# Kernel tuning notes

Hardware: AMD Instinct MI355X
Metric: run time of the kernel (lower is better)

Reference implementation:

```python
import jax, jax.numpy as jnp
import numpy as np


def _pairwise_dist(x, y):
    # x: [b, n, d], y: [b, n, d] -> squared L2 distances [b, n, n]
    xx = jnp.sum(x * x, axis=-1)  # [b, n]
    yy = jnp.sum(y * y, axis=-1)  # [b, n]
    zz = jnp.einsum('bnd,bmd->bnm', x, y)  # [b, n, n]
    return xx[:, :, None] + yy[:, None, :] - 2.0 * zz


def setup_inputs() -> dict:
    key = jax.random.key(0)
    k1, k2 = jax.random.split(key)
    bs, n, d = 4, 8192, 3
    x = jax.random.normal(k1, (bs, n, d), dtype=jnp.float32)
    y = jax.random.normal(k2, (bs, n, d), dtype=jnp.float32)
    return {"x": x, "y": y}


def reference(x, y):
    bs, n_points, _ = x.shape
    dist1 = jnp.sqrt(_pairwise_dist(x, y))  # [b, n, n]
    values1 = jnp.min(dist1, axis=2)        # [b, n] min over y for each x point
    dist2 = jnp.sqrt(_pairwise_dist(y, x))
    values2 = jnp.min(dist2, axis=2)        # min over x for each y point
    a = jnp.sum(values1, axis=1) / n_points
    b = jnp.sum(values2, axis=1) / n_points
    return jnp.sum(a) / bs + jnp.sum(b) / bs
```

## Files before the change

kernel.cpp:

```cpp
#include <hip/hip_runtime.h>
#include <stdint.h>

typedef _Float16 half8 __attribute__((ext_vector_type(8)));
typedef float f32x16 __attribute__((ext_vector_type(16)));

#define NPTS 8192
#define BS 4
#define TOTQ 65536
#define TPB 256
#define NS 4
#define QPB 512
#define NCHUNK 4
#define SLICE (NPTS / NS)

__device__ __forceinline__ float4 f4min(float4 a, float4 b) {
    return make_float4(fminf(a.x, b.x), fminf(a.y, b.y), fminf(a.z, b.z), fminf(a.w, b.w));
}

__device__ __forceinline__ void mk_afrag(float p0, float p1, float p2,
                                         half8* ag0, half8* ag1) {
    _Float16 h0 = (_Float16)p0, h1 = (_Float16)p1, h2 = (_Float16)p2;
    _Float16 l0 = (_Float16)(p0 - (float)h0);
    _Float16 l1 = (_Float16)(p1 - (float)h1);
    _Float16 l2 = (_Float16)(p2 - (float)h2);
    _Float16 t2 = (_Float16)-2.0f;
    _Float16 m0 = t2 * h0, m1 = t2 * h1, m2 = t2 * h2;
    _Float16 n0 = t2 * l0, n1 = t2 * l1, n2 = t2 * l2;
    _Float16 one = (_Float16)1.0f, zz = (_Float16)0.0f;
    *ag0 = (half8){m0, m1, m2, n0, n1, n2, m0, m1};
    *ag1 = (half8){m2, one, one, n0, n1, n2, zz, zz};
}

__device__ __forceinline__ void mk_bfrag(float p0, float p1, float p2,
                                         half8* bg0, half8* bg1) {
    float nt = p0 * p0 + p1 * p1 + p2 * p2;
    _Float16 h0 = (_Float16)p0, h1 = (_Float16)p1, h2 = (_Float16)p2;
    _Float16 l0 = (_Float16)(p0 - (float)h0);
    _Float16 l1 = (_Float16)(p1 - (float)h1);
    _Float16 l2 = (_Float16)(p2 - (float)h2);
    _Float16 nh = (_Float16)nt;
    _Float16 nl = (_Float16)(nt - (float)nh);
    _Float16 zz = (_Float16)0.0f;
    *bg0 = (half8){h0, h1, h2, h0, h1, h2, l0, l1};
    *bg1 = (half8){l2, nh, nl, l0, l1, l2, zz, zz};
}

__global__ __launch_bounds__(TPB, 2) void mfma_min_kernel(const float* __restrict__ x,
                                                          const float* __restrict__ y,
                                                          float* __restrict__ partial) {
    __shared__ __align__(16) char lds[2][16384];
    const int tid = threadIdx.x;
    const int wave = tid >> 6;
    const int l = tid & 63;
    const int chunkid = blockIdx.x / NS;
    const int s = blockIdx.x % NS;
    const int qbase = chunkid * QPB;
    const int dir = qbase >> 15;
    const int b = (qbase >> 13) & 3;
    const int qpt = qbase & (BS * NPTS - 1);
    const int tpt = b * NPTS + s * SLICE;
    const float* qsrc = (dir == 0) ? x : y;
    const float* tsrc = (dir == 0) ? y : x;

    half8 afr0, afr1, afr2, afr3;
    {
        const int row = l & 31;
#define MKA(AF, a)                                                                          \
        {                                                                                   \
            const float* p = qsrc + (size_t)(qpt + (wave * 4 + (a)) * 32 + row) * 3;        \
            half8 g0, g1;                                                                   \
            mk_afrag(p[0], p[1], p[2], &g0, &g1);                                           \
            AF = (l < 32) ? g0 : g1;                                                        \
        }
        MKA(afr0, 0) MKA(afr1, 1) MKA(afr2, 2) MKA(afr3, 3)
#undef MKA
    }

    f32x16 mrun0, mrun1, mrun2, mrun3, zc;
#pragma unroll
    for (int r = 0; r < 16; ++r) {
        mrun0[r] = 3.4e38f; mrun1[r] = 3.4e38f;
        mrun2[r] = 3.4e38f; mrun3[r] = 3.4e38f;
        zc[r] = 0.0f;
    }

    float2 rA, rB, rC;
#define BLOAD(c)                                                                            \
    {                                                                                       \
        const float2* p = (const float2*)(tsrc + (size_t)(tpt + (c) * 512 + tid * 2) * 3);  \
        rA = p[0]; rB = p[1]; rC = p[2];                                                    \
    }
#define BPACK(buf)                                                                          \
    {                                                                                       \
        const int t0 = tid * 2;                                                             \
        const int base = (t0 >> 5) * 1024;                                                  \
        const int r0 = (t0 & 31) * 16;                                                      \
        half8 g0, g1;                                                                       \
        mk_bfrag(rA.x, rA.y, rB.x, &g0, &g1);                                               \
        *(half8*)(&lds[buf][base + r0]) = g0;                                               \
        *(half8*)(&lds[buf][base + 512 + r0]) = g1;                                         \
        mk_bfrag(rB.y, rC.x, rC.y, &g0, &g1);                                               \
        *(half8*)(&lds[buf][base + r0 + 16]) = g0;                                          \
        *(half8*)(&lds[buf][base + 512 + r0 + 16]) = g1;                                    \
    }

#define AGROUP(AF, MR, BB0, BB1)                                                            \
    {                                                                                       \
        f32x16 d0 = __builtin_amdgcn_mfma_f32_32x32x16_f16(AF, BB0, zc, 0, 0, 0);           \
        f32x16 d1 = __builtin_amdgcn_mfma_f32_32x32x16_f16(AF, BB1, zc, 0, 0, 0);           \
        _Pragma("unroll")                                                                   \
        for (int r = 0; r < 16; ++r)                                                        \
            MR[r] = fminf(fminf(MR[r], d0[r]), d1[r]);                          \
    }

#define COMPUTE(BB0, BB1)                                                                   \
    AGROUP(afr0, mrun0, BB0, BB1)                                                           \
    AGROUP(afr1, mrun1, BB0, BB1)                                                           \
    AGROUP(afr2, mrun2, BB0, BB1)                                                           \
    AGROUP(afr3, mrun3, BB0, BB1)

    BLOAD(0)
    BPACK(0)
    __syncthreads();

    int cur = 0;
#pragma unroll 1
    for (int c = 0; c < NCHUNK; ++c) {
        if (c + 1 < NCHUNK) BLOAD(c + 1)
        const char* B = lds[cur];
        half8 bA0 = *(const half8*)(B + l * 16);
        half8 bA1 = *(const half8*)(B + 1024 + l * 16);
        half8 bB0, bB1;
#pragma unroll 1
        for (int p = 0; p < 8; p += 2) {
            bB0 = *(const half8*)(B + (p + 1) * 2048 + l * 16);
            bB1 = *(const half8*)(B + (p + 1) * 2048 + 1024 + l * 16);
            COMPUTE(bA0, bA1);
            int pn = (p + 2) & 7;
            bA0 = *(const half8*)(B + pn * 2048 + l * 16);
            bA1 = *(const half8*)(B + pn * 2048 + 1024 + l * 16);
            COMPUTE(bB0, bB1);
        }
        if (c + 1 < NCHUNK) {
            BPACK(cur ^ 1)
            __syncthreads();
            cur ^= 1;
        }
    }
#undef BLOAD
#undef BPACK
#undef COMPUTE
#undef AGROUP

    __syncthreads();
    float* ep = (float*)(&lds[0][0]);
    const int hi4 = (l >> 5) * 4;
    const int col = l & 31;

#define EPASS(AA, MR)                                                                       \
    {                                                                                       \
        _Pragma("unroll")                                                                   \
        for (int r = 0; r < 16; ++r) {                                                      \
            int row = (r & 3) + 8 * (r >> 2) + hi4;                                         \
            ep[wave * 1152 + row * 36 + col] = MR[r];                                       \
        }                                                                                   \
    }                                                                                       \
    __syncthreads();                                                                        \
    if (tid < 128) {                                                                        \
        const float4* rp = (const float4*)(ep + (tid >> 5) * 1152 + (tid & 31) * 36);       \
        float4 a01 = f4min(rp[0], rp[1]), a23 = f4min(rp[2], rp[3]);                        \
        float4 a45 = f4min(rp[4], rp[5]), a67 = f4min(rp[6], rp[7]);                        \
        float4 t = f4min(f4min(a01, a23), f4min(a45, a67));                                 \
        float m = fminf(fminf(t.x, t.y), fminf(t.z, t.w));                                  \
        partial[(size_t)s * TOTQ + qbase + (tid >> 5) * 128 + (AA) * 32 + (tid & 31)] = m;  \
    }                                                                                       \
    __syncthreads();

    EPASS(0, mrun0)
    EPASS(1, mrun1)
    EPASS(2, mrun2)
    EPASS(3, mrun3)
#undef EPASS
}

__global__ __launch_bounds__(TPB) void combine_mfma_kernel(const float* __restrict__ partial,
                                                           const float* __restrict__ x,
                                                           const float* __restrict__ y,
                                                           float* __restrict__ bsum) {
    int q = blockIdx.x * TPB + threadIdx.x;
    int dir = q >> 15;
    int pidx = q & (BS * NPTS - 1);
    const float* src = (dir == 0) ? x : y;
    float p0 = src[pidx * 3 + 0], p1 = src[pidx * 3 + 1], p2 = src[pidx * 3 + 2];
    float nq = p0 * p0 + p1 * p1 + p2 * p2;

    float m = partial[q];
#pragma unroll
    for (int s = 1; s < NS; ++s)
        m = fminf(m, partial[(size_t)s * TOTQ + q]);
    float d = sqrtf(fmaxf(m + nq, 0.0f));
    __shared__ float red[TPB];
    red[threadIdx.x] = d;
    __syncthreads();
    for (int off = TPB / 2; off > 0; off >>= 1) {
        if (threadIdx.x < off) red[threadIdx.x] += red[threadIdx.x + off];
        __syncthreads();
    }
    if (threadIdx.x == 0) bsum[blockIdx.x] = red[0];
}

__global__ __launch_bounds__(TPB) void final_kernel(const float* __restrict__ bsum,
                                                    float* __restrict__ out) {
    __shared__ float red[TPB];
    red[threadIdx.x] = bsum[threadIdx.x];
    __syncthreads();
    for (int off = TPB / 2; off > 0; off >>= 1) {
        if (threadIdx.x < off) red[threadIdx.x] += red[threadIdx.x + off];
        __syncthreads();
    }
    if (threadIdx.x == 0) out[0] = red[0] * (1.0f / 32768.0f);
}

#define QPT 8
#define QPBF (TPB * QPT)
#define NGROUP (TOTQ / QPBF)
#define FNS 8

__global__ __launch_bounds__(TPB) void pack_kernel(const float* __restrict__ x,
                                                   const float* __restrict__ y,
                                                   float4* __restrict__ px,
                                                   float4* __restrict__ py) {
    int i = blockIdx.x * TPB + threadIdx.x;
    if (i < BS * NPTS) {
        float x0 = x[i * 3 + 0], x1 = x[i * 3 + 1], x2 = x[i * 3 + 2];
        px[i] = make_float4(x0, x1, x2, x0 * x0 + x1 * x1 + x2 * x2);
        float y0 = y[i * 3 + 0], y1 = y[i * 3 + 1], y2 = y[i * 3 + 2];
        py[i] = make_float4(y0, y1, y2, y0 * y0 + y1 * y1 + y2 * y2);
    }
}

__global__ __launch_bounds__(TPB) void chamfer_min_kernel(const float4* __restrict__ px,
                                                          const float4* __restrict__ py,
                                                          float* __restrict__ partial) {
    constexpr int SLICEF = NPTS / FNS;
    __shared__ float4 tile[SLICEF];
    const int t = threadIdx.x;
    const int g = blockIdx.x / FNS;
    const int s = blockIdx.x % FNS;
    const int dir = g >> 4;
    const int b = (g >> 2) & 3;
    const int chunk = g & 3;
    const float4* q  = (dir == 0 ? px : py) + b * NPTS + chunk * QPBF;
    const float4* tg = (dir == 0 ? py : px) + b * NPTS + s * SLICEF;
    float a0[QPT], a1[QPT], a2[QPT], qq[QPT], mv[QPT];
#pragma unroll
    for (int i = 0; i < QPT; ++i) {
        float4 v = q[i * TPB + t];
        a0[i] = -2.0f * v.x; a1[i] = -2.0f * v.y; a2[i] = -2.0f * v.z;
        qq[i] = v.w; mv[i] = 3.4e38f;
    }
#pragma unroll
    for (int i = 0; i < SLICEF / TPB; ++i)
        tile[i * TPB + t] = tg[i * TPB + t];
    __syncthreads();
#pragma unroll 2
    for (int j = 0; j < SLICEF; j += 2) {
        float4 v0 = tile[j], v1 = tile[j + 1];
#pragma unroll
        for (int i = 0; i < QPT; ++i) {
            float d0 = fmaf(a2[i], v0.z, fmaf(a1[i], v0.y, fmaf(a0[i], v0.x, v0.w)));
            float d1 = fmaf(a2[i], v1.z, fmaf(a1[i], v1.y, fmaf(a0[i], v1.x, v1.w)));
            mv[i] = fminf(fminf(mv[i], d0), d1);
        }
    }
    const int qg0 = g * QPBF;
#pragma unroll
    for (int i = 0; i < QPT; ++i)
        partial[(size_t)s * TOTQ + qg0 + i * TPB + t] = mv[i] + qq[i];
}

__global__ __launch_bounds__(TPB) void combine_kernel(const float* __restrict__ partial,
                                                      float* __restrict__ bsum) {
    int idx = blockIdx.x * TPB + threadIdx.x;
    float m = 3.4e38f;
#pragma unroll
    for (int s = 0; s < FNS; ++s)
        m = fminf(m, partial[(size_t)s * TOTQ + idx]);
    float d = sqrtf(fmaxf(m, 0.0f));
    __shared__ float red[TPB];
    red[threadIdx.x] = d;
    __syncthreads();
    for (int off = TPB / 2; off > 0; off >>= 1) {
        if (threadIdx.x < off) red[threadIdx.x] += red[threadIdx.x + off];
        __syncthreads();
    }
    if (threadIdx.x == 0) bsum[blockIdx.x] = red[0];
}

extern "C" void kernel_launch(void* const* d_in, const int* in_sizes, int n_in,
                              void* d_out, int out_size, void* d_ws, size_t ws_size,
                              hipStream_t stream) {
    const float* x = (const float*)d_in[0];
    const float* y = (const float*)d_in[1];
    float* out = (float*)d_out;
    char* ws = (char*)d_ws;

    const size_t off_bs = (size_t)NS * TOTQ * 4;
    const size_t need = off_bs + 1024;

    if (ws_size >= need) {
        float* partial = (float*)ws;
        float* bsum = (float*)(ws + off_bs);
        hipLaunchKernelGGL(mfma_min_kernel, dim3((TOTQ / QPB) * NS), dim3(TPB), 0, stream,
                           x, y, partial);
        hipLaunchKernelGGL(combine_mfma_kernel, dim3(TOTQ / TPB), dim3(TPB), 0, stream,
                           partial, x, y, bsum);
        hipLaunchKernelGGL(final_kernel, dim3(1), dim3(TPB), 0, stream, bsum, out);
    } else {
        float4* px = (float4*)ws;
        float4* py = (float4*)(ws + 512 * 1024);
        float* partial = (float*)(ws + 1024 * 1024);
        float* bsum = (float*)(ws + 1024 * 1024 + (size_t)FNS * TOTQ * 4);
        hipLaunchKernelGGL(pack_kernel, dim3((BS * NPTS + TPB - 1) / TPB), dim3(TPB), 0, stream,
                           x, y, px, py);
        hipLaunchKernelGGL(chamfer_min_kernel, dim3(NGROUP * FNS), dim3(TPB), 0, stream,
                           px, py, partial);
        hipLaunchKernelGGL(combine_kernel, dim3(TOTQ / TPB), dim3(TPB), 0, stream,
                           partial, bsum);
        hipLaunchKernelGGL(final_kernel, dim3(1), dim3(TPB), 0, stream, bsum, out);
    }
}
```

Before: 29.00 us.

## Stage entire target slice into LDS upfront instead of double-buffered chunks

Replaces the four-chunk double-buffered LDS pipeline with a single prologue that loads and packs all 2048 target points into a 64KB LDS buffer. Global loads for two chunks are interleaved with packing, then one barrier precedes an uninterrupted 32-step MFMA loop. This removes the per-chunk barriers and load/pack work inside the compute loop. In exchange, LDS use per block rises from 32KB to 64KB, which may limit blocks per CU to two or fewer. Global load latency is also exposed up front instead of overlapped with compute.

```diff
diff --git a/kernel.cpp b/kernel.cpp
--- a/kernel.cpp
+++ b/kernel.cpp
@@ -10,7 +10,6 @@
 #define TPB 256
 #define NS 4
 #define QPB 512
-#define NCHUNK 4
 #define SLICE (NPTS / NS)
 
 __device__ __forceinline__ float4 f4min(float4 a, float4 b) {
@@ -48,7 +47,7 @@
 __global__ __launch_bounds__(TPB, 2) void mfma_min_kernel(const float* __restrict__ x,
                                                           const float* __restrict__ y,
                                                           float* __restrict__ partial) {
-    __shared__ __align__(16) char lds[2][16384];
+    __shared__ __align__(16) char lds[65536];
     const int tid = threadIdx.x;
     const int wave = tid >> 6;
     const int l = tid & 63;
@@ -84,25 +83,36 @@
         zc[r] = 0.0f;
     }
 
-    float2 rA, rB, rC;
-#define BLOAD(c)                                                                            \
+#define BLOADs(c, RA, RB, RC)                                                               \
     {                                                                                       \
         const float2* p = (const float2*)(tsrc + (size_t)(tpt + (c) * 512 + tid * 2) * 3);  \
-        rA = p[0]; rB = p[1]; rC = p[2];                                                    \
-    }
-#define BPACK(buf)                                                                          \
+        RA = p[0]; RB = p[1]; RC = p[2];                                                    \
+    }
+#define BPACKs(c, RA, RB, RC)                                                               \
     {                                                                                       \
-        const int t0 = tid * 2;                                                             \
+        const int t0 = (c) * 512 + tid * 2;                                                 \
         const int base = (t0 >> 5) * 1024;                                                  \
         const int r0 = (t0 & 31) * 16;                                                      \
         half8 g0, g1;                                                                       \
-        mk_bfrag(rA.x, rA.y, rB.x, &g0, &g1);                                               \
-        *(half8*)(&lds[buf][base + r0]) = g0;                                               \
-        *(half8*)(&lds[buf][base + 512 + r0]) = g1;                                         \
-        mk_bfrag(rB.y, rC.x, rC.y, &g0, &g1);                                               \
-        *(half8*)(&lds[buf][base + r0 + 16]) = g0;                                          \
-        *(half8*)(&lds[buf][base + 512 + r0 + 16]) = g1;                                    \
-    }
+        mk_bfrag(RA.x, RA.y, RB.x, &g0, &g1);                                               \
+        *(half8*)(&lds[base + r0]) = g0;                                                    \
+        *(half8*)(&lds[base + 512 + r0]) = g1;                                              \
+        mk_bfrag(RB.y, RC.x, RC.y, &g0, &g1);                                               \
+        *(half8*)(&lds[base + r0 + 16]) = g0;                                               \
+        *(half8*)(&lds[base + 512 + r0 + 16]) = g1;                                         \
+    }
+    {
+        float2 rA0, rB0, rC0, rA1, rB1, rC1;
+        BLOADs(0, rA0, rB0, rC0)
+        BLOADs(1, rA1, rB1, rC1)
+        BPACKs(0, rA0, rB0, rC0)
+        BLOADs(2, rA0, rB0, rC0)
+        BPACKs(1, rA1, rB1, rC1)
+        BLOADs(3, rA1, rB1, rC1)
+        BPACKs(2, rA0, rB0, rC0)
+        BPACKs(3, rA1, rB1, rC1)
+    }
+    __syncthreads();
 
 #define AGROUP(AF, MR, BB0, BB1)                                                            \
     {                                                                                       \
@@ -119,41 +129,29 @@
     AGROUP(afr2, mrun2, BB0, BB1)                                                           \
     AGROUP(afr3, mrun3, BB0, BB1)
 
-    BLOAD(0)
-    BPACK(0)
-    __syncthreads();
-
-    int cur = 0;
-#pragma unroll 1
-    for (int c = 0; c < NCHUNK; ++c) {
-        if (c + 1 < NCHUNK) BLOAD(c + 1)
-        const char* B = lds[cur];
+    {
+        const char* B = lds;
         half8 bA0 = *(const half8*)(B + l * 16);
         half8 bA1 = *(const half8*)(B + 1024 + l * 16);
         half8 bB0, bB1;
 #pragma unroll 1
-        for (int p = 0; p < 8; p += 2) {
+        for (int p = 0; p < 32; p += 2) {
             bB0 = *(const half8*)(B + (p + 1) * 2048 + l * 16);
             bB1 = *(const half8*)(B + (p + 1) * 2048 + 1024 + l * 16);
             COMPUTE(bA0, bA1);
-            int pn = (p + 2) & 7;
+            int pn = (p + 2) & 31;
             bA0 = *(const half8*)(B + pn * 2048 + l * 16);
             bA1 = *(const half8*)(B + pn * 2048 + 1024 + l * 16);
             COMPUTE(bB0, bB1);
         }
-        if (c + 1 < NCHUNK) {
-            BPACK(cur ^ 1)
-            __syncthreads();
-            cur ^= 1;
-        }
-    }
-#undef BLOAD
-#undef BPACK
+    }
+#undef BLOADs
+#undef BPACKs
 #undef COMPUTE
 #undef AGROUP
 
     __syncthreads();
-    float* ep = (float*)(&lds[0][0]);
+    float* ep = (float*)(&lds[0]);
     const int hi4 = (l >> 5) * 4;
     const int col = l & 31;
 
```

Measured after the change: 30.51 us. +5.2%, slower.
